# Optimization experiments

Hardware: AMD Instinct MI355X
Metric: run time of the kernel (lower is better)

## Reference

```python
import jax, jax.numpy as jnp
import numpy as np

EPS = 1e-5


def ternarize(w):
    # TWN: delta = 0.7*mean|w|; alpha = mean of |w| over entries above delta
    delta = 0.7 * jnp.mean(jnp.abs(w))
    mask = (jnp.abs(w) > delta).astype(w.dtype)
    alpha = jnp.sum(jnp.abs(w) * mask) / jnp.maximum(jnp.sum(mask), 1.0)
    q = alpha * jnp.sign(w) * mask
    # straight-through estimator (matches torch `w + (q - w).detach()`)
    return w + jax.lax.stop_gradient(q - w)


def conv2d(x, w, stride, pad):
    # x: NCHW, w: OIHW
    return jax.lax.conv_general_dilated(
        x, w, window_strides=(stride, stride), padding=[(pad, pad), (pad, pad)],
        dimension_numbers=("NCHW", "OIHW", "NCHW"))


def batchnorm(x, gamma, beta, mean, var):
    # inference-mode BN over channel dim of NCHW
    inv = gamma / jnp.sqrt(var + EPS)
    return x * inv[None, :, None, None] + (beta - mean * inv)[None, :, None, None]


def setup_inputs() -> dict:
    key = jax.random.key(0)
    ks = jax.random.split(key, 12)
    d = {
        "x": jax.random.normal(ks[0], (64, 3, 224, 224), jnp.float32),
        "w1": jax.random.normal(ks[1], (32, 3, 3, 3), jnp.float32) * 0.1,
        "g1": jnp.ones((32,), jnp.float32), "b1": jnp.zeros((32,), jnp.float32),
        "m1": jax.random.normal(ks[2], (32,), jnp.float32) * 0.1,
        "v1": jax.random.uniform(ks[3], (32,), jnp.float32, 0.5, 1.5),
        "w2": jax.random.normal(ks[4], (64, 32, 3, 3), jnp.float32) * 0.05,
        "g2": jnp.ones((64,), jnp.float32), "b2": jnp.zeros((64,), jnp.float32),
        "m2": jax.random.normal(ks[5], (64,), jnp.float32) * 0.1,
        "v2": jax.random.uniform(ks[6], (64,), jnp.float32, 0.5, 1.5),
        "w3": jax.random.normal(ks[7], (128, 64, 3, 3), jnp.float32) * 0.05,
        "g3": jnp.ones((128,), jnp.float32), "b3": jnp.zeros((128,), jnp.float32),
        "m3": jax.random.normal(ks[8], (128,), jnp.float32) * 0.1,
        "v3": jax.random.uniform(ks[9], (128,), jnp.float32, 0.5, 1.5),
        "wl": jax.random.normal(ks[10], (10, 128), jnp.float32) * 0.1,
        "bl": jax.random.normal(ks[11], (10,), jnp.float32) * 0.01,
    }
    return d


def reference(x, w1, g1, b1, m1, v1, w2, g2, b2, m2, v2,
              w3, g3, b3, m3, v3, wl, bl):
    h = jax.nn.relu(batchnorm(conv2d(x, ternarize(w1), 2, 1), g1, b1, m1, v1))
    h = jax.nn.relu(batchnorm(conv2d(h, ternarize(w2), 1, 1), g2, b2, m2, v2))
    h = jax.nn.relu(batchnorm(conv2d(h, ternarize(w3), 2, 1), g3, b3, m3, v3))
    h = jnp.mean(h, axis=(2, 3))  # AdaptiveAvgPool2d((1,1)) + flatten -> [N,128]
    return h @ ternarize(wl).T + bl
```

## Files before the change

kernel.cpp:

```cpp
#include <hip/hip_runtime.h>
#include <cstddef>

typedef __attribute__((ext_vector_type(8))) short short8;
typedef __attribute__((ext_vector_type(4))) float floatx4;

__device__ __forceinline__ unsigned short f2bf(float f) {
  union { float f; unsigned u; } v; v.f = f;
  const unsigned r = v.u + 0x7fffu + ((v.u >> 16) & 1u);
  return (unsigned short)(r >> 16);
}

__device__ __forceinline__ float block_reduce_sum(float v, float* sm) {
#pragma unroll
  for (int off = 32; off > 0; off >>= 1) v += __shfl_down(v, off, 64);
  const int lane = threadIdx.x & 63, wid = threadIdx.x >> 6;
  __syncthreads();
  if (lane == 0) sm[wid] = v;
  __syncthreads();
  if (threadIdx.x == 0) {
    float t = 0.f;
    const int nw = (blockDim.x + 63) >> 6;
    for (int i = 0; i < nw; ++i) t += sm[i];
    sm[0] = t;
  }
  __syncthreads();
  return sm[0];
}

__device__ __forceinline__ void tsel(int t, const float* w0, const float* w1,
                                     const float* w2, const float* w3, int n0,
                                     int n1, int n2, int n3,
                                     const float*& w, int& n) {
  w = (t == 0) ? w0 : (t == 1) ? w1 : (t == 2) ? w2 : w3;
  n = (t == 0) ? n0 : (t == 1) ? n1 : (t == 2) ? n2 : n3;
}

__global__ __launch_bounds__(256) void tern_phase1(
    const float* w0, const float* w1, const float* w2, const float* w3,
    int n0, int n1, int n2, int n3, float* __restrict__ red) {
  __shared__ float sm[8];
  const float* w; int n;
  tsel(blockIdx.y, w0, w1, w2, w3, n0, n1, n2, n3, w, n);
  if ((int)blockIdx.x * 256 >= n) return;
  const int i = blockIdx.x * 256 + threadIdx.x;
  float s = (i < n) ? fabsf(w[i]) : 0.f;
  s = block_reduce_sum(s, sm);
  if (threadIdx.x == 0) atomicAdd(&red[blockIdx.y * 4 + 0], s);
}

__global__ __launch_bounds__(256) void tern_phase2(
    const float* w0, const float* w1, const float* w2, const float* w3,
    int n0, int n1, int n2, int n3, float* __restrict__ red,
    unsigned short* __restrict__ bp1, unsigned short* __restrict__ bp2,
    unsigned short* __restrict__ bp3, float* __restrict__ ql) {
  __shared__ float sm[8];
  const float* w; int n;
  const int by = blockIdx.y;
  tsel(by, w0, w1, w2, w3, n0, n1, n2, n3, w, n);
  if ((int)blockIdx.x * 256 >= n) return;
  const float delta = 0.7f * red[by * 4 + 0] / (float)n;
  const int i = blockIdx.x * 256 + threadIdx.x;
  float c = 0.f, a = 0.f;
  float wv = 0.f;
  if (i < n) {
    wv = w[i];
    const float av = fabsf(wv);
    if (av > delta) { c = 1.f; a = av; }
  }
  if (i < n) {
    const float sgnf = (wv > delta) ? 1.f : (wv < -delta ? -1.f : 0.f);
    const unsigned short sgnb =
        (wv > delta) ? 0x3F80u : (wv < -delta ? 0xBF80u : 0u);
    if (by == 0) {
      const int k = i % 27, oc = i / 27;
      bp1[((size_t)(k >> 3) * 32 + oc) * 8 + (k & 7)] = sgnb;
    } else if (by == 1) {
      const int k = (i % 9) * 32 + (i % 288) / 9;
      bp2[((size_t)(k >> 3) * 64 + i / 288) * 8 + (k & 7)] = sgnb;
    } else if (by == 2) {
      const int k = (i % 9) * 64 + (i % 576) / 9;
      bp3[((size_t)(k >> 3) * 128 + i / 576) * 8 + (k & 7)] = sgnb;
    } else {
      ql[i] = sgnf;
    }
  }
  c = block_reduce_sum(c, sm);
  a = block_reduce_sum(a, sm);
  if (threadIdx.x == 0) {
    atomicAdd(&red[by * 4 + 1], c);
    atomicAdd(&red[by * 4 + 2], a);
  }
}

__global__ void bnfold_all(
    const float* g1, const float* b1, const float* m1, const float* v1,
    const float* g2, const float* b2, const float* m2, const float* v2,
    const float* g3, const float* b3, const float* m3, const float* v3,
    float* s1, float* bb1, float* s2, float* bb2, float* s3, float* bb3,
    const float* __restrict__ red) {
  const int i = threadIdx.x;
  if (i < 32) {
    const float inv = g1[i] / sqrtf(v1[i] + 1e-5f);
    const float a = red[2] / fmaxf(red[1], 1.f);
    s1[i] = a * inv; bb1[i] = b1[i] - m1[i] * inv;
  } else if (i < 96) {
    const int c = i - 32;
    const float inv = g2[c] / sqrtf(v2[c] + 1e-5f);
    const float a = red[6] / fmaxf(red[5], 1.f);
    s2[c] = a * inv; bb2[c] = b2[c] - m2[c] * inv;
  } else if (i < 224) {
    const int c = i - 96;
    const float inv = g3[c] / sqrtf(v3[c] + 1e-5f);
    const float a = red[10] / fmaxf(red[9], 1.f);
    s3[c] = a * inv; bb3[c] = b3[c] - m3[c] * inv;
  }
}

__global__ __launch_bounds__(256) void conv1_mfma(
    const float* __restrict__ x, const unsigned short* __restrict__ bp1,
    const float* __restrict__ s1, const float* __restrict__ bb1,
    unsigned short* __restrict__ y) {
  __shared__ float xs[3 * 17 * 33];
  __shared__ unsigned short im[128 * 40];
  const int n = blockIdx.y;
  const int oh0 = (blockIdx.x / 7) * 8, ow0 = (blockIdx.x % 7) * 16;
  const int t = threadIdx.x;
  const int wave = t >> 6, lane = t & 63, quad = lane >> 4, l16 = lane & 15;

  const int ihb = oh0 * 2 - 1, iwb = ow0 * 2 - 1;
  for (int i = t; i < 1683; i += 256) {
    const int ic = i / 561, r2 = i % 561;
    const int pr = r2 / 33, pc = r2 % 33;
    const int ih = ihb + pr, iw = iwb + pc;
    float v = 0.f;
    if ((unsigned)ih < 224u && (unsigned)iw < 224u)
      v = x[((size_t)n * 3 + ic) * 50176 + (size_t)ih * 224 + iw];
    xs[i] = v;
  }
  __syncthreads();

#pragma unroll
  for (int cc = 0; cc < 2; ++cc) {
    const int c = cc * 256 + t;
    const int px = c >> 2, seg = c & 3;
    const int ohl = px >> 4, owl = px & 15;
    unsigned u[4];
#pragma unroll
    for (int jj = 0; jj < 4; ++jj) {
      unsigned short lo = 0, hi = 0;
      const int k0 = seg * 8 + 2 * jj, k1 = k0 + 1;
      if (k0 < 27) {
        const int ic = k0 / 9, tp = k0 % 9;
        lo = f2bf(xs[(ic * 17 + ohl * 2 + tp / 3) * 33 + owl * 2 + tp % 3]);
      }
      if (k1 < 27) {
        const int ic = k1 / 9, tp = k1 % 9;
        hi = f2bf(xs[(ic * 17 + ohl * 2 + tp / 3) * 33 + owl * 2 + tp % 3]);
      }
      u[jj] = (unsigned)lo | ((unsigned)hi << 16);
    }
    *(uint4*)(&im[px * 40 + seg * 8]) = make_uint4(u[0], u[1], u[2], u[3]);
  }

  short8 bfr[2];
#pragma unroll
  for (int nf = 0; nf < 2; ++nf)
    bfr[nf] = *(const short8*)(bp1 + ((size_t)quad * 32 + nf * 16 + l16) * 8);

  floatx4 acc[2][2];
#pragma unroll
  for (int mi = 0; mi < 2; ++mi) {
    acc[mi][0] = (floatx4){0.f, 0.f, 0.f, 0.f};
    acc[mi][1] = (floatx4){0.f, 0.f, 0.f, 0.f};
  }
  __syncthreads();

#pragma unroll
  for (int mi = 0; mi < 2; ++mi) {
    const int pxb = (wave * 2 + mi) * 16;
    const short8 a = *(const short8*)(&im[(pxb + l16) * 40 + quad * 8]);
#pragma unroll
    for (int nf = 0; nf < 2; ++nf)
      acc[mi][nf] = __builtin_amdgcn_mfma_f32_16x16x32_bf16(
          a, bfr[nf], acc[mi][nf], 0, 0, 0);
  }

  float sc[2], bs[2];
#pragma unroll
  for (int nf = 0; nf < 2; ++nf) {
    sc[nf] = s1[nf * 16 + l16];
    bs[nf] = bb1[nf * 16 + l16];
  }
#pragma unroll
  for (int mi = 0; mi < 2; ++mi) {
    const int oh = oh0 + wave * 2 + mi;
#pragma unroll
    for (int r = 0; r < 4; ++r) {
      const int ow = ow0 + quad * 4 + r;
      const size_t base = (((size_t)n * 112 + oh) * 112 + ow) * 32;
#pragma unroll
      for (int nf = 0; nf < 2; ++nf) {
        const float vv = fmaxf(acc[mi][nf][r] * sc[nf] + bs[nf], 0.f);
        y[base + nf * 16 + l16] = f2bf(vv);
      }
    }
  }
}

__global__ __launch_bounds__(256) void conv2_halo(
    const unsigned short* __restrict__ xin,
    const unsigned short* __restrict__ bp,
    const float* __restrict__ scale, const float* __restrict__ bias,
    unsigned short* __restrict__ yout) {
  constexpr int PH = 10, PW = 18;
  __shared__ unsigned short patch[4 * PH * PW * 8];
  const int t = threadIdx.x;
  const int img = blockIdx.z;
  const int toh = blockIdx.x / 7, tow = blockIdx.x % 7;
  const int wave = t >> 6, lane = t & 63, quad = lane >> 4, l16 = lane & 15;
  const int oh0 = toh * 8, ow0 = tow * 16;

  for (int c = t; c < PH * PW * 4; c += 256) {
    const int pix = c >> 2, seg = c & 3;
    const int pi = pix / PW, pj = pix % PW;
    const int ih = oh0 - 1 + pi, iw = ow0 - 1 + pj;
    uint4 v = make_uint4(0u, 0u, 0u, 0u);
    if ((unsigned)ih < 112u && (unsigned)iw < 112u)
      v = *(const uint4*)(xin + (((size_t)img * 112 + ih) * 112 + iw) * 32 +
                          seg * 8);
    *(uint4*)(&patch[((seg * PH + pi) * PW + pj) * 8]) = v;
  }

  floatx4 acc[2][4];
#pragma unroll
  for (int mf = 0; mf < 2; ++mf)
#pragma unroll
    for (int nf = 0; nf < 4; ++nf) acc[mf][nf] = (floatx4){0.f, 0.f, 0.f, 0.f};

  short8 bcur[4], bnxt[4];
#pragma unroll
  for (int nf = 0; nf < 4; ++nf)
    bcur[nf] = *(const short8*)(bp + ((size_t)quad * 64 + nf * 16 + l16) * 8);
  __syncthreads();

#pragma unroll
  for (int tap = 0; tap < 9; ++tap) {
    const int kh = tap / 3, kw = tap % 3;
    if (tap + 1 < 9) {
      const int kg = (tap + 1) * 4 + quad;
#pragma unroll
      for (int nf = 0; nf < 4; ++nf)
        bnxt[nf] = *(const short8*)(bp + ((size_t)kg * 64 + nf * 16 + l16) * 8);
    }
#pragma unroll
    for (int mf = 0; mf < 2; ++mf) {
      const int pi = (wave * 2 + mf) + kh;
      const short8 a = *(const short8*)(
          &patch[((quad * PH + pi) * PW + l16 + kw) * 8]);
#pragma unroll
      for (int nf = 0; nf < 4; ++nf)
        acc[mf][nf] = __builtin_amdgcn_mfma_f32_16x16x32_bf16(
            a, bcur[nf], acc[mf][nf], 0, 0, 0);
    }
#pragma unroll
    for (int nf = 0; nf < 4; ++nf) bcur[nf] = bnxt[nf];
  }

  float sc[4], bs[4];
#pragma unroll
  for (int nf = 0; nf < 4; ++nf) {
    sc[nf] = scale[nf * 16 + l16];
    bs[nf] = bias[nf * 16 + l16];
  }
#pragma unroll
  for (int mf = 0; mf < 2; ++mf) {
    const int oh = oh0 + wave * 2 + mf;
#pragma unroll
    for (int r = 0; r < 4; ++r) {
      const int ow = ow0 + quad * 4 + r;
      const size_t base = (((size_t)img * 112 + oh) * 112 + ow) * 64;
#pragma unroll
      for (int nf = 0; nf < 4; ++nf) {
        const float vv = fmaxf(acc[mf][nf][r] * sc[nf] + bs[nf], 0.f);
        yout[base + nf * 16 + l16] = f2bf(vv);
      }
    }
  }
}

__global__ __launch_bounds__(256, 5) void conv3_pool(
    const unsigned short* __restrict__ act2,
    const unsigned short* __restrict__ bp3,
    const float* __restrict__ s3, const float* __restrict__ bb3,
    float* __restrict__ pooled) {
  __shared__ unsigned short c2p[4 * 17 * 18 * 8];
  __shared__ float pbuf[128];
  const int t = threadIdx.x;
  const int img = blockIdx.y;
  const int ty = blockIdx.x / 7, tx = blockIdx.x % 7;
  const int o3h0 = ty * 8, o3w0 = tx * 8;
  const int wave = t >> 6, lane = t & 63, quad = lane >> 4, l16 = lane & 15;

  int a3off[4];
#pragma unroll
  for (int mf = 0; mf < 4; ++mf) {
    const int px = mf * 16 + l16;
    a3off[mf] = ((quad * 17 + (px >> 3) * 2) * 18 + (px & 7)) * 8;
  }

  floatx4 acc3[4][2];
#pragma unroll
  for (int mf = 0; mf < 4; ++mf) {
    acc3[mf][0] = (floatx4){0.f, 0.f, 0.f, 0.f};
    acc3[mf][1] = (floatx4){0.f, 0.f, 0.f, 0.f};
  }

  const int h0 = o3h0 * 2 - 1, w0 = o3w0 * 2 - 1;
#pragma unroll
  for (int h = 0; h < 2; ++h) {
    if (h) __syncthreads();
    for (int c = t; c < 17 * 17 * 4; c += 256) {
      const int pix = c >> 2, seg = c & 3;
      const int pi = pix / 17, pj = pix % 17;
      const int ih = h0 + pi, iw = w0 + pj;
      uint4 v = make_uint4(0u, 0u, 0u, 0u);
      if ((unsigned)ih < 112u && (unsigned)iw < 112u)
        v = *(const uint4*)(act2 + (((size_t)img * 112 + ih) * 112 + iw) * 64 +
                            h * 32 + seg * 8);
      const int slot = (pj >> 1) + (pj & 1) * 9;
      *(uint4*)(&c2p[((seg * 17 + pi) * 18 + slot) * 8]) = v;
    }
    __syncthreads();
#pragma unroll
    for (int tap = 0; tap < 9; ++tap) {
      const int kh = tap / 3, kw = tap % 3;
      const int kg = tap * 8 + h * 4 + quad;
      const short8 b0 = *(const short8*)(
          bp3 + ((size_t)kg * 128 + wave * 32 + l16) * 8);
      const short8 b1 = *(const short8*)(
          bp3 + ((size_t)kg * 128 + wave * 32 + 16 + l16) * 8);
      const int toff = (kh * 18 + (kw >> 1) + (kw & 1) * 9) * 8;
#pragma unroll
      for (int mf = 0; mf < 4; ++mf) {
        const short8 a = *(const short8*)(&c2p[a3off[mf] + toff]);
        acc3[mf][0] = __builtin_amdgcn_mfma_f32_16x16x32_bf16(
            a, b0, acc3[mf][0], 0, 0, 0);
        acc3[mf][1] = __builtin_amdgcn_mfma_f32_16x16x32_bf16(
            a, b1, acc3[mf][1], 0, 0, 0);
      }
    }
  }

#pragma unroll
  for (int nf = 0; nf < 2; ++nf) {
    const int ch = wave * 32 + nf * 16 + l16;
    const float sc = s3[ch], bs = bb3[ch];
    float s = 0.f;
#pragma unroll
    for (int mf = 0; mf < 4; ++mf)
#pragma unroll
      for (int r = 0; r < 4; ++r)
        s += fmaxf(acc3[mf][nf][r] * sc + bs, 0.f);
    s += __shfl_xor(s, 16);
    s += __shfl_xor(s, 32);
    if (lane < 16) pbuf[ch] = s;
  }
  __syncthreads();
  if (t < 128) atomicAdd(&pooled[(size_t)img * 128 + t], pbuf[t]);
}

__global__ void linear_kernel(const float* __restrict__ pooled,
                              const float* __restrict__ ql,
                              const float* __restrict__ bl,
                              const float* __restrict__ red,
                              float* __restrict__ out) {
  const int idx = blockIdx.x * blockDim.x + threadIdx.x;
  if (idx >= 64 * 10) return;
  const int n = idx / 10, o = idx % 10;
  const float* p = pooled + (size_t)n * 128;
  const float* w = ql + (size_t)o * 128;
  float s = 0.f;
#pragma unroll 4
  for (int c = 0; c < 128; ++c) s += p[c] * w[c];
  const float alpha_l = red[14] / fmaxf(red[13], 1.f);
  out[idx] = s * (alpha_l / 3136.f) + bl[o];
}

extern "C" void kernel_launch(void* const* d_in, const int* in_sizes, int n_in,
                              void* d_out, int out_size, void* d_ws,
                              size_t ws_size, hipStream_t stream) {
  const float* x  = (const float*)d_in[0];
  const float* w1 = (const float*)d_in[1];
  const float* g1 = (const float*)d_in[2];
  const float* b1 = (const float*)d_in[3];
  const float* m1 = (const float*)d_in[4];
  const float* v1 = (const float*)d_in[5];
  const float* w2 = (const float*)d_in[6];
  const float* g2 = (const float*)d_in[7];
  const float* b2 = (const float*)d_in[8];
  const float* m2 = (const float*)d_in[9];
  const float* v2 = (const float*)d_in[10];
  const float* w3 = (const float*)d_in[11];
  const float* g3 = (const float*)d_in[12];
  const float* b3 = (const float*)d_in[13];
  const float* m3 = (const float*)d_in[14];
  const float* v3 = (const float*)d_in[15];
  const float* wl = (const float*)d_in[16];
  const float* bl = (const float*)d_in[17];
  float* out = (float*)d_out;

  float* Wf = (float*)d_ws;
  float* red = Wf;
  float* pooled = red + 16;
  float* bp1f = pooled + 8192;
  float* ql = bp1f + 512;
  float* s1 = ql + 1280;  float* bb1 = s1 + 32;
  float* s2 = bb1 + 32;   float* bb2 = s2 + 64;
  float* s3 = bb2 + 64;   float* bb3 = s3 + 128;
  unsigned short* bp1 = (unsigned short*)bp1f;
  unsigned short* Us = (unsigned short*)(bb3 + 128);
  unsigned short* bp2 = Us;
  unsigned short* bp3 = bp2 + 18432;
  unsigned short* act1 = bp3 + 73728;
  unsigned short* act2 = act1 + 25690112;

  hipMemsetAsync(red, 0, (16 + 8192 + 512) * sizeof(float), stream);
  tern_phase1<<<dim3(288, 4), 256, 0, stream>>>(w1, w2, w3, wl, 864, 18432,
                                                73728, 1280, red);
  tern_phase2<<<dim3(288, 4), 256, 0, stream>>>(w1, w2, w3, wl, 864, 18432,
                                                73728, 1280, red, bp1, bp2,
                                                bp3, ql);
  bnfold_all<<<1, 256, 0, stream>>>(g1, b1, m1, v1, g2, b2, m2, v2, g3, b3,
                                    m3, v3, s1, bb1, s2, bb2, s3, bb3, red);

  conv1_mfma<<<dim3(98, 64), 256, 0, stream>>>(x, bp1, s1, bb1, act1);
  conv2_halo<<<dim3(98, 1, 64), 256, 0, stream>>>(act1, bp2, s2, bb2, act2);
  conv3_pool<<<dim3(49, 64), 256, 0, stream>>>(act2, bp3, s3, bb3, pooled);
  linear_kernel<<<3, 256, 0, stream>>>(pooled, ql, bl, red, out);
}
```

Measured before the change: 258.5 us.

## Permute conv2 output channels for packed stores and reorder conv3 LDS fill

The conv2 weight packing now permutes output channels so each lane owns four consecutive channels. The epilogue can then write four bf16 values as one 8-byte store instead of four scattered 2-byte stores. The conv3 patch loader also changes its thread-to-element mapping so consecutive threads write consecutive LDS slots, trading coalescing of global reads across channel segments for more contiguous LDS writes. The channel permutation has to stay consistent between packing, the scale/bias indexing and the output layout.

New measurement: 288.4 us. 1.12x slower.

```diff
diff --git a/kernel.cpp b/kernel.cpp
--- a/kernel.cpp
+++ b/kernel.cpp
@@ -76,7 +76,9 @@
       bp1[((size_t)(k >> 3) * 32 + oc) * 8 + (k & 7)] = sgnb;
     } else if (by == 1) {
       const int k = (i % 9) * 32 + (i % 288) / 9;
-      bp2[((size_t)(k >> 3) * 64 + i / 288) * 8 + (k & 7)] = sgnb;
+      const int och = i / 288;
+      const int p = ((och & 3) << 4) | (och >> 2);
+      bp2[((size_t)(k >> 3) * 64 + p) * 8 + (k & 7)] = sgnb;
     } else if (by == 2) {
       const int k = (i % 9) * 64 + (i % 576) / 9;
       bp3[((size_t)(k >> 3) * 128 + i / 576) * 8 + (k & 7)] = sgnb;
@@ -269,8 +271,8 @@
   float sc[4], bs[4];
 #pragma unroll
   for (int nf = 0; nf < 4; ++nf) {
-    sc[nf] = scale[nf * 16 + l16];
-    bs[nf] = bias[nf * 16 + l16];
+    sc[nf] = scale[l16 * 4 + nf];
+    bs[nf] = bias[l16 * 4 + nf];
   }
 #pragma unroll
   for (int mf = 0; mf < 2; ++mf) {
@@ -278,12 +280,14 @@
 #pragma unroll
     for (int r = 0; r < 4; ++r) {
       const int ow = ow0 + quad * 4 + r;
-      const size_t base = (((size_t)img * 112 + oh) * 112 + ow) * 64;
-#pragma unroll
-      for (int nf = 0; nf < 4; ++nf) {
-        const float vv = fmaxf(acc[mf][nf][r] * sc[nf] + bs[nf], 0.f);
-        yout[base + nf * 16 + l16] = f2bf(vv);
-      }
+      const size_t base = (((size_t)img * 112 + oh) * 112 + ow) * 64 + l16 * 4;
+      const float v0 = fmaxf(acc[mf][0][r] * sc[0] + bs[0], 0.f);
+      const float v1 = fmaxf(acc[mf][1][r] * sc[1] + bs[1], 0.f);
+      const float v2 = fmaxf(acc[mf][2][r] * sc[2] + bs[2], 0.f);
+      const float v3 = fmaxf(acc[mf][3][r] * sc[3] + bs[3], 0.f);
+      const unsigned u0 = (unsigned)f2bf(v0) | ((unsigned)f2bf(v1) << 16);
+      const unsigned u1 = (unsigned)f2bf(v2) | ((unsigned)f2bf(v3) << 16);
+      *(uint2*)(yout + base) = make_uint2(u0, u1);
     }
   }
 }
@@ -320,15 +324,15 @@
   for (int h = 0; h < 2; ++h) {
     if (h) __syncthreads();
     for (int c = t; c < 17 * 17 * 4; c += 256) {
-      const int pix = c >> 2, seg = c & 3;
-      const int pi = pix / 17, pj = pix % 17;
+      const int seg = c / 289, rem = c % 289;
+      const int pi = rem / 17, sl = rem % 17;
+      const int pj = (sl < 9) ? sl * 2 : (sl - 9) * 2 + 1;
       const int ih = h0 + pi, iw = w0 + pj;
       uint4 v = make_uint4(0u, 0u, 0u, 0u);
       if ((unsigned)ih < 112u && (unsigned)iw < 112u)
         v = *(const uint4*)(act2 + (((size_t)img * 112 + ih) * 112 + iw) * 64 +
                             h * 32 + seg * 8);
-      const int slot = (pj >> 1) + (pj & 1) * 9;
-      *(uint4*)(&c2p[((seg * 17 + pi) * 18 + slot) * 8]) = v;
+      *(uint4*)(&c2p[((seg * 17 + pi) * 18 + sl) * 8]) = v;
     }
     __syncthreads();
 #pragma unroll
```
